# Kernel optimization log

Hardware: AMD Instinct MI355X
Metric: run time of the kernel (lower is better)

The kernel has to match this reference:

```python
import jax, jax.numpy as jnp
import numpy as np

MODEL_DIM = 2048
NUM_HEADS = 16
NUM_KV_HEADS = 4
HEAD_DIM = MODEL_DIM // NUM_HEADS  # 128
ROPE_BASE = 10000.0
LOCAL_WINDOW = 1024
EPS = 1.1920929e-07  # torch.finfo(float32).eps, F.rms_norm default
NEG = -1e30


def setup_inputs() -> dict:
    key = jax.random.key(0)
    ks = jax.random.split(key, 5)
    s = 0.02
    return {
        "x": jax.random.normal(ks[0], (1, 4096, MODEL_DIM), jnp.float32),
        "Wq": jax.random.normal(ks[1], (MODEL_DIM, MODEL_DIM), jnp.float32) * s,
        "Wk": jax.random.normal(ks[2], (NUM_KV_HEADS * HEAD_DIM, MODEL_DIM), jnp.float32) * s,
        "Wv": jax.random.normal(ks[3], (NUM_KV_HEADS * HEAD_DIM, MODEL_DIM), jnp.float32) * s,
        "Wo": jax.random.normal(ks[4], (MODEL_DIM, MODEL_DIM), jnp.float32) * s,
    }


def _rms_norm(x):
    return x * jax.lax.rsqrt(jnp.mean(x * x, axis=-1, keepdims=True) + EPS)


def _rope_tables(seqlen, dtype):
    inv_freq = 1.0 / (ROPE_BASE ** (jnp.arange(0, HEAD_DIM, 2, dtype=jnp.float32) / HEAD_DIM))
    freqs = jnp.arange(seqlen, dtype=jnp.float32)[:, None] * inv_freq[None, :]  # [S, hd/2]
    return jnp.cos(freqs).astype(dtype), jnp.sin(freqs).astype(dtype)


def _apply_rope(x, cos, sin):
    # x: [B, H, S, hd]; cos/sin: [S, hd/2]
    half = x.shape[-1] // 2
    x1, x2 = x[..., :half], x[..., half:]
    c = cos[None, None, :, :]
    s = sin[None, None, :, :]
    return jnp.concatenate((x1 * c + x2 * s, x2 * c - x1 * s), axis=-1)


def reference(x, Wq, Wk, Wv, Wo):
    B, S, _ = x.shape
    G = NUM_HEADS // NUM_KV_HEADS
    q = (x @ Wq.T).reshape(B, S, NUM_HEADS, HEAD_DIM).transpose(0, 2, 1, 3)
    k = (x @ Wk.T).reshape(B, S, NUM_KV_HEADS, HEAD_DIM).transpose(0, 2, 1, 3)
    v = (x @ Wv.T).reshape(B, S, NUM_KV_HEADS, HEAD_DIM).transpose(0, 2, 1, 3)
    q = _rms_norm(q)
    k = _rms_norm(k)
    cos, sin = _rope_tables(S, q.dtype)
    q = _apply_rope(q, cos, sin)
    k = _apply_rope(k, cos, sin)
    # GQA: expand kv heads to match query heads
    k = jnp.repeat(k, G, axis=1)  # [B, H, S, hd]
    v = jnp.repeat(v, G, axis=1)
    scale = 1.0 / np.sqrt(HEAD_DIM)
    scores = jnp.einsum("bhqd,bhkd->bhqk", q, k) * scale  # [B, H, S, S]
    idx = jnp.arange(S)
    causal = idx[None, :] <= idx[:, None]
    in_window = idx[None, :] > idx[:, None] - LOCAL_WINDOW
    allowed = causal & in_window  # [S, S]
    scores = jnp.where(allowed[None, None, :, :], scores, NEG)
    probs = jax.nn.softmax(scores, axis=-1)
    y = jnp.einsum("bhqk,bhkd->bhqd", probs, v)  # [B, H, S, hd]
    y = y.transpose(0, 2, 1, 3).reshape(B, S, MODEL_DIM)
    return y @ Wo.T
```

## Files before the change

kernel.cpp:

```cpp
#include <hip/hip_runtime.h>

typedef short bf16x8 __attribute__((ext_vector_type(8)));
typedef short short4v __attribute__((ext_vector_type(4)));
typedef float f32x4 __attribute__((ext_vector_type(4)));

__device__ __forceinline__ ushort f2b(float f) {
  union { float f; unsigned u; } v; v.f = f;
  unsigned r = v.u + 0x7FFF + ((v.u >> 16) & 1);
  return (ushort)(r >> 16);
}
__device__ __forceinline__ float b2f(ushort u) {
  union { unsigned u; float f; } v; v.u = ((unsigned)u) << 16;
  return v.f;
}
__device__ __forceinline__ unsigned cvtpk(float lo, float hi) {
  unsigned r;
  asm volatile("v_cvt_pk_bf16_f32 %0, %1, %2" : "=v"(r) : "v"(lo), "v"(hi));
  return r;
}
__device__ __forceinline__ f32x4 mfma16(bf16x8 a, bf16x8 b, f32x4 c) {
  return __builtin_amdgcn_mfma_f32_16x16x32_bf16(a, b, c, 0, 0, 0);
}

#define GLD_LDS16(g, l) \
  __builtin_amdgcn_global_load_lds((const __attribute__((address_space(1))) void*)(g), \
                                   (__attribute__((address_space(3))) void*)(l), 16, 0, 0)

__global__ __launch_bounds__(256) void cast_bf16(const float* __restrict__ in,
                                                 ushort* __restrict__ out, int n4) {
  int i = blockIdx.x * 256 + threadIdx.x;
  if (i >= n4) return;
  float4 f = ((const float4*)in)[i];
  ushort4 u;
  u.x = f2b(f.x); u.y = f2b(f.y); u.z = f2b(f.z); u.w = f2b(f.w);
  ((ushort4*)out)[i] = u;
}

__global__ void rope_tables_k(float* __restrict__ cosT, float* __restrict__ sinT) {
  int s = blockIdx.x, i = threadIdx.x;
  float inv = powf(10000.0f, -(float)i * (1.0f / 64.0f));
  float f = (float)s * inv;
  cosT[s * 64 + i] = cosf(f);
  sinT[s * 64 + i] = sinf(f);
}

template <bool BF16OUT>
__global__ __launch_bounds__(256) void gemm_bt(const ushort* __restrict__ A,
                                               const ushort* __restrict__ B,
                                               void* __restrict__ Cout,
                                               int M, int N, int K) {
  __shared__ __align__(16) ushort As[128 * 32];
  __shared__ __align__(16) ushort Bs[128 * 32];
  const int t = threadIdx.x;
  const int lane = t & 63, w = t >> 6;
  const int wr = w >> 1, wc = w & 1;
  const int l15 = lane & 15, l4 = lane >> 4;
  const long m0 = (long)blockIdx.y * 128, n0 = (long)blockIdx.x * 128;
  f32x4 acc[4][4] = {};
  const int srow = t >> 2, scol = (t & 3) * 8;
  const ushort* ga = A + (m0 + srow) * K + scol;
  const ushort* gb = B + (n0 + srow) * K + scol;
  for (int k0 = 0; k0 < K; k0 += 32) {
    GLD_LDS16(ga,          &As[t * 8]);
    GLD_LDS16(ga + 64 * K, &As[2048 + t * 8]);
    GLD_LDS16(gb,          &Bs[t * 8]);
    GLD_LDS16(gb + 64 * K, &Bs[2048 + t * 8]);
    ga += 32; gb += 32;
    asm volatile("s_waitcnt vmcnt(0)" ::: "memory");
    __syncthreads();
    bf16x8 af[4], bfr[4];
#pragma unroll
    for (int i = 0; i < 4; ++i) {
      af[i]  = *(const bf16x8*)(&As[(wr * 64 + i * 16 + l15) * 32 + l4 * 8]);
      bfr[i] = *(const bf16x8*)(&Bs[(wc * 64 + i * 16 + l15) * 32 + l4 * 8]);
    }
#pragma unroll
    for (int i = 0; i < 4; ++i)
#pragma unroll
      for (int j = 0; j < 4; ++j)
        acc[i][j] = mfma16(af[i], bfr[j], acc[i][j]);
    __syncthreads();
  }
#pragma unroll
  for (int i = 0; i < 4; ++i) {
#pragma unroll
    for (int j = 0; j < 4; ++j) {
      long mrow = m0 + wr * 64 + i * 16 + l4 * 4;
      long ncol = n0 + wc * 64 + j * 16 + l15;
#pragma unroll
      for (int r = 0; r < 4; ++r) {
        if constexpr (BF16OUT)
          ((ushort*)Cout)[(mrow + r) * N + ncol] = f2b(acc[i][j][r]);
        else
          ((float*)Cout)[(mrow + r) * N + ncol] = acc[i][j][r];
      }
    }
  }
}

__global__ __launch_bounds__(256) void postproc_k(const ushort* __restrict__ qkvb,
                                                  const float* __restrict__ cosT,
                                                  const float* __restrict__ sinT,
                                                  ushort* __restrict__ qb,
                                                  ushort* __restrict__ kb,
                                                  ushort* __restrict__ vtb) {
  const int lane = threadIdx.x & 63;
  const int s = blockIdx.x * 4 + (threadIdx.x >> 6);
  const int h = blockIdx.y;
  const int colbase = (h < 16) ? h * 128 : (h < 20 ? 2048 + (h - 16) * 128
                                                   : 2560 + (h - 20) * 128);
  const ushort* row = qkvb + (long)s * 3072 + colbase;
  float x1 = b2f(row[lane]), x2 = b2f(row[lane + 64]);
  if (h >= 20) {
    int kvh = h - 20;
    vtb[(long)(kvh * 128 + lane) * 4096 + s]      = f2b(x1);
    vtb[(long)(kvh * 128 + lane + 64) * 4096 + s] = f2b(x2);
    return;
  }
  float ss = x1 * x1 + x2 * x2;
#pragma unroll
  for (int m = 1; m < 64; m <<= 1) ss += __shfl_xor(ss, m);
  float rn = rsqrtf(ss * (1.0f / 128.0f) + 1.1920929e-07f);
  float c = cosT[s * 64 + lane], sn = sinT[s * 64 + lane];
  float x1n = x1 * rn, x2n = x2 * rn;
  float o1 = x1n * c + x2n * sn;
  float o2 = x2n * c - x1n * sn;
  if (h < 16) {
    const float scq = 0.08838834764831845f;
    ushort* dst = qb + ((long)h * 4096 + s) * 128;
    dst[lane] = f2b(o1 * scq);
    dst[lane + 64] = f2b(o2 * scq);
  } else {
    ushort* dst = kb + ((long)(h - 16) * 4096 + s) * 128;
    dst[lane] = f2b(o1);
    dst[lane + 64] = f2b(o2);
  }
}

__global__ __launch_bounds__(512) void attn_k(const ushort* __restrict__ qb,
                                              const ushort* __restrict__ kb,
                                              const ushort* __restrict__ vtb,
                                              ushort* __restrict__ yb) {
  __shared__ __align__(16) ushort lds[32768];
  const int t = threadIdx.x;
  const int lane = t & 63, w = t >> 6;
  const int l15 = lane & 15, l4 = lane >> 4;
  const int q0 = ((int)gridDim.x - 1 - (int)blockIdx.x) * 128;
  const int h = blockIdx.y, kvh = h >> 2;
  const int qw = q0 + w * 16;
  const int q = qw + l15;
  const int swz = l15 & 7;

  const ushort* Qp = qb + ((long)h * 4096 + q) * 128 + l4 * 8;
  bf16x8 qf[4];
#pragma unroll
  for (int c = 0; c < 4; ++c) qf[c] = *(const bf16x8*)(Qp + c * 32);

  const ushort* Kg = kb + (long)kvh * 4096 * 128;
  const ushort* Vg = vtb + (long)kvh * 128 * 4096;

  int kb_lo = q0 - 1023; if (kb_lo < 0) kb_lo = 0; kb_lo &= ~63;
  const int nt = (q0 + 127 - kb_lo) / 64 + 1;

  const int lbuA = (0 * 8 + w) * 512 + lane * 8;
  const int lbuB = (1 * 8 + w) * 512 + lane * 8;
  const int krA = lbuA >> 7, kcA = ((lbuA >> 3) & 15) ^ (krA & 7);
  const int krB = lbuB >> 7, kcB = ((lbuB >> 3) & 15) ^ (krB & 7);
  const int vrA = lbuA >> 6, vcA = ((lbuA >> 3) & 7) ^ (vrA & 7);
  const int vrB = lbuB >> 6, vcB = ((lbuB >> 3) & 7) ^ (vrB & 7);

#define STAGE(kbs, b)                                                        \
  do {                                                                       \
    ushort* Kl_ = &lds[(b) * 16384];                                         \
    ushort* Vl_ = &lds[(b) * 16384 + 8192];                                  \
    GLD_LDS16(Kg + (long)((kbs) + krA) * 128 + kcA * 8, Kl_ + lbuA);         \
    GLD_LDS16(Kg + (long)((kbs) + krB) * 128 + kcB * 8, Kl_ + lbuB);         \
    GLD_LDS16(Vg + (long)vrA * 4096 + (kbs) + vcA * 8, Vl_ + lbuA);          \
    GLD_LDS16(Vg + (long)vrB * 4096 + (kbs) + vcB * 8, Vl_ + lbuB);          \
  } while (0)

  f32x4 o[8] = {};
  float mrun = -1e30f, lrun = 0.0f;

  STAGE(kb_lo, 0);
  asm volatile("s_waitcnt vmcnt(0)" ::: "memory");
  __syncthreads();

  for (int ti = 0; ti < nt; ++ti) {
    const int kbs = kb_lo + ti * 64;
    const int cur = ti & 1;
    if (ti + 1 < nt) STAGE(kbs + 64, cur ^ 1);

    if (kbs + 63 >= qw - 1023 && kbs <= qw + 15) {
      const ushort* Kl = &lds[cur * 16384];
      const ushort* Vl = &lds[cur * 16384 + 8192];

      f32x4 sc[4];
#pragma unroll
      for (int st = 0; st < 4; ++st) {
        sc[st] = f32x4{0.f, 0.f, 0.f, 0.f};
        const ushort* kr = Kl + (st * 16 + l15) * 128;
#pragma unroll
        for (int c = 0; c < 4; ++c)
          sc[st] = mfma16(*(const bf16x8*)(kr + (((c * 4 + l4) ^ swz) * 8)), qf[c], sc[st]);
      }

      float s[16];
#pragma unroll
      for (int st = 0; st < 4; ++st)
#pragma unroll
        for (int r = 0; r < 4; ++r) {
          const int ki = kbs + st * 16 + l4 * 4 + r;
          s[st * 4 + r] = (ki <= q && ki > q - 1024) ? sc[st][r] : -1e30f;
        }

      float m0a = fmaxf(fmaxf(s[0], s[1]), fmaxf(s[2], s[3]));
      float m1a = fmaxf(fmaxf(s[4], s[5]), fmaxf(s[6], s[7]));
      float m2a = fmaxf(fmaxf(s[8], s[9]), fmaxf(s[10], s[11]));
      float m3a = fmaxf(fmaxf(s[12], s[13]), fmaxf(s[14], s[15]));
      float mx = fmaxf(fmaxf(m0a, m1a), fmaxf(m2a, m3a));
      mx = fmaxf(mx, __shfl_xor(mx, 16));
      mx = fmaxf(mx, __shfl_xor(mx, 32));

      float mn;
      if (__all(mx <= mrun + 8.0f)) {
        mn = mrun;
      } else {
        mn = fmaxf(mrun, mx);
        const float corr = __expf(mrun - mn);
        mrun = mn;
#pragma unroll
        for (int db = 0; db < 8; ++db)
#pragma unroll
          for (int r = 0; r < 4; ++r) o[db][r] *= corr;
        lrun *= corr;
      }

      float p[16];
#pragma unroll
      for (int j = 0; j < 16; ++j) p[j] = __expf(s[j] - mn);
      float ps = ((p[0] + p[1]) + (p[2] + p[3])) + ((p[4] + p[5]) + (p[6] + p[7]));
      ps += ((p[8] + p[9]) + (p[10] + p[11])) + ((p[12] + p[13]) + (p[14] + p[15]));
      ps += __shfl_xor(ps, 16);
      ps += __shfl_xor(ps, 32);
      lrun += ps;

      union { unsigned u[4]; bf16x8 v; } pa, pb;
      pa.u[0] = cvtpk(p[0], p[1]);   pa.u[1] = cvtpk(p[2], p[3]);
      pa.u[2] = cvtpk(p[4], p[5]);   pa.u[3] = cvtpk(p[6], p[7]);
      pb.u[0] = cvtpk(p[8], p[9]);   pb.u[1] = cvtpk(p[10], p[11]);
      pb.u[2] = cvtpk(p[12], p[13]); pb.u[3] = cvtpk(p[14], p[15]);

      const int co = 4 * (l4 & 1);
      const int c0 = (l4 >> 1) ^ swz, c1 = (2 + (l4 >> 1)) ^ swz;
      const int c2 = (4 + (l4 >> 1)) ^ swz, c3 = (6 + (l4 >> 1)) ^ swz;
#pragma unroll
      for (int db = 0; db < 8; ++db) {
        const ushort* vr = Vl + (db * 16 + l15) * 64;
        short4v a0 = *(const short4v*)(vr + c0 * 8 + co);
        short4v a1 = *(const short4v*)(vr + c1 * 8 + co);
        bf16x8 va = __builtin_shufflevector(a0, a1, 0, 1, 2, 3, 4, 5, 6, 7);
        o[db] = mfma16(va, pa.v, o[db]);
        short4v b0 = *(const short4v*)(vr + c2 * 8 + co);
        short4v b1 = *(const short4v*)(vr + c3 * 8 + co);
        bf16x8 vb = __builtin_shufflevector(b0, b1, 0, 1, 2, 3, 4, 5, 6, 7);
        o[db] = mfma16(vb, pb.v, o[db]);
      }
    }
    __syncthreads();
  }

  const float inv = 1.0f / lrun;
#pragma unroll
  for (int db = 0; db < 8; ++db)
#pragma unroll
    for (int r = 0; r < 4; ++r)
      yb[(long)q * 2048 + h * 128 + db * 16 + l4 * 4 + r] = f2b(o[db][r] * inv);
}

extern "C" void kernel_launch(void* const* d_in, const int* in_sizes, int n_in,
                              void* d_out, int out_size, void* d_ws, size_t ws_size,
                              hipStream_t stream) {
  (void)in_sizes; (void)n_in; (void)out_size; (void)ws_size;
  const float* x  = (const float*)d_in[0];
  const float* Wq = (const float*)d_in[1];
  const float* Wk = (const float*)d_in[2];
  const float* Wv = (const float*)d_in[3];
  const float* Wo = (const float*)d_in[4];
  const long S = 4096;
  ushort* ws   = (ushort*)d_ws;
  ushort* xb   = ws;
  ushort* wqkv = xb + S * 2048;
  ushort* wob  = wqkv + 3072L * 2048;
  ushort* qkvb = wob + 2048L * 2048;
  ushort* qb   = qkvb + S * 3072;
  ushort* kbuf = qb + S * 2048;
  ushort* vtb  = kbuf + 4L * 4096 * 128;
  ushort* yb   = vtb + 4L * 128 * 4096;
  float* cosT  = (float*)(yb + S * 2048);
  float* sinT  = cosT + S * 64;

  cast_bf16<<<dim3(8192), 256, 0, stream>>>(x, xb, (int)(S * 2048 / 4));
  cast_bf16<<<dim3(4096), 256, 0, stream>>>(Wq, wqkv, 2048 * 2048 / 4);
  cast_bf16<<<dim3(1024), 256, 0, stream>>>(Wk, wqkv + 2048L * 2048, 512 * 2048 / 4);
  cast_bf16<<<dim3(1024), 256, 0, stream>>>(Wv, wqkv + 2560L * 2048, 512 * 2048 / 4);
  cast_bf16<<<dim3(4096), 256, 0, stream>>>(Wo, wob, 2048 * 2048 / 4);

  gemm_bt<true><<<dim3(24, 32), 256, 0, stream>>>(xb, wqkv, qkvb, 4096, 3072, 2048);
  rope_tables_k<<<dim3(4096), 64, 0, stream>>>(cosT, sinT);
  postproc_k<<<dim3(1024, 24), 256, 0, stream>>>(qkvb, cosT, sinT, qb, kbuf, vtb);
  attn_k<<<dim3(32, 16), 512, 0, stream>>>(qb, kbuf, vtb, yb);
  gemm_bt<false><<<dim3(16, 32), 256, 0, stream>>>(yb, wob, d_out, 4096, 2048, 2048);
}
```

Baseline: 238.6 us.

## Replace GEMMs with 8-wave pipelined kernel and retile attention LDS layout

Swaps the simple 128x128 GEMM for a 512-thread, 256-wide tiled GEMM. It double-buffers LDS with async global-to-LDS loads interleaved with MFMA phases, uses s_setprio, and remaps workgroups across XCDs. The attention kernel's K/V LDS layout becomes MFMA-fragment-ordered, so fragments load as contiguous 16-byte reads instead of swizzled split loads. V transpose storage is permuted to match, and masking is skipped for fully in-window tiles. This targets GEMM latency stalls and LDS read overhead, at the cost of complex, fragile layout coupling between postproc and attention.

Result: faster. 225.1 us (-5.6%).

```diff
diff --git a/kernel.cpp b/kernel.cpp
--- a/kernel.cpp
+++ b/kernel.cpp
@@ -1,7 +1,6 @@
 #include <hip/hip_runtime.h>
 
 typedef short bf16x8 __attribute__((ext_vector_type(8)));
-typedef short short4v __attribute__((ext_vector_type(4)));
 typedef float f32x4 __attribute__((ext_vector_type(4)));
 
 __device__ __forceinline__ ushort f2b(float f) {
@@ -44,58 +43,124 @@
   sinT[s * 64 + i] = sinf(f);
 }
 
-template <bool BF16OUT>
-__global__ __launch_bounds__(256) void gemm_bt(const ushort* __restrict__ A,
-                                               const ushort* __restrict__ B,
-                                               void* __restrict__ Cout,
-                                               int M, int N, int K) {
-  __shared__ __align__(16) ushort As[128 * 32];
-  __shared__ __align__(16) ushort Bs[128 * 32];
+template <int BM, int BN, bool BF16OUT>
+__global__ __launch_bounds__(512, 2) void gemm8p(const ushort* __restrict__ A,
+                                                 const ushort* __restrict__ B,
+                                                 void* __restrict__ Cout,
+                                                 int M, int N, int K) {
+  constexpr int AF = BM / 64;
+  constexpr int BF = BN / 64;
+  constexpr int MFR = BM / 32;
+  constexpr int LA = BM / 128;
+  constexpr int LB = BN / 128;
+  constexpr int ASZ = BM * 32;
+  constexpr int BSZ = BN * 32;
+  __shared__ __align__(16) ushort lds[4 * (ASZ + BSZ)];
   const int t = threadIdx.x;
   const int lane = t & 63, w = t >> 6;
-  const int wr = w >> 1, wc = w & 1;
+  const int wr = w & 1, wc = w >> 1;
   const int l15 = lane & 15, l4 = lane >> 4;
-  const long m0 = (long)blockIdx.y * 128, n0 = (long)blockIdx.x * 128;
-  f32x4 acc[4][4] = {};
-  const int srow = t >> 2, scol = (t & 3) * 8;
-  const ushort* ga = A + (m0 + srow) * K + scol;
-  const ushort* gb = B + (n0 + srow) * K + scol;
-  for (int k0 = 0; k0 < K; k0 += 32) {
-    GLD_LDS16(ga,          &As[t * 8]);
-    GLD_LDS16(ga + 64 * K, &As[2048 + t * 8]);
-    GLD_LDS16(gb,          &Bs[t * 8]);
-    GLD_LDS16(gb + 64 * K, &Bs[2048 + t * 8]);
-    ga += 32; gb += 32;
-    asm volatile("s_waitcnt vmcnt(0)" ::: "memory");
-    __syncthreads();
-    bf16x8 af[4], bfr[4];
-#pragma unroll
-    for (int i = 0; i < 4; ++i) {
-      af[i]  = *(const bf16x8*)(&As[(wr * 64 + i * 16 + l15) * 32 + l4 * 8]);
-      bfr[i] = *(const bf16x8*)(&Bs[(wc * 64 + i * 16 + l15) * 32 + l4 * 8]);
-    }
-#pragma unroll
-    for (int i = 0; i < 4; ++i)
-#pragma unroll
-      for (int j = 0; j < 4; ++j)
-        acc[i][j] = mfma16(af[i], bfr[j], acc[i][j]);
-    __syncthreads();
-  }
-#pragma unroll
-  for (int i = 0; i < 4; ++i) {
-#pragma unroll
-    for (int j = 0; j < 4; ++j) {
-      long mrow = m0 + wr * 64 + i * 16 + l4 * 4;
-      long ncol = n0 + wc * 64 + j * 16 + l15;
+  const int nbn = N / BN;
+  const int nwg = (int)gridDim.x;
+  int bid = (int)blockIdx.x;
+  bid = (bid & 7) * (nwg >> 3) + (bid >> 3);
+  const long m0 = (long)(bid / nbn) * BM;
+  const long n0 = (long)(bid % nbn) * BN;
+  const int nk = K >> 6;
+  const int rdl = (l4 * 16 + l15) * 8;
+
+  f32x4 acc[MFR][BF] = {};
+  bf16x8 af[AF], bf[BF];
+
+#define STA(tile, ks)                                                          \
+  do {                                                                         \
+    const int tt_ = (tile) < nk ? (tile) : nk - 1;                             \
+    _Pragma("unroll") for (int c = 0; c < LA; ++c) {                           \
+      const int us_ = t * 8 + c * 4096;                                        \
+      const int row_ = (us_ >> 9) * 16 + ((us_ >> 3) & 15);                    \
+      const int col_ = ((us_ >> 7) & 3) * 8;                                   \
+      GLD_LDS16(A + (m0 + row_) * K + tt_ * 64 + (ks) * 32 + col_,             \
+                &lds[(((tile) & 1) * 2 + (ks)) * ASZ + us_]);                  \
+    }                                                                          \
+  } while (0)
+#define STB(tile, ks)                                                          \
+  do {                                                                         \
+    const int tt_ = (tile) < nk ? (tile) : nk - 1;                             \
+    _Pragma("unroll") for (int c = 0; c < LB; ++c) {                           \
+      const int us_ = t * 8 + c * 4096;                                        \
+      const int row_ = (us_ >> 9) * 16 + ((us_ >> 3) & 15);                    \
+      const int col_ = ((us_ >> 7) & 3) * 8;                                   \
+      GLD_LDS16(B + (n0 + row_) * K + tt_ * 64 + (ks) * 32 + col_,             \
+                &lds[4 * ASZ + (((tile) & 1) * 2 + (ks)) * BSZ + us_]);        \
+    }                                                                          \
+  } while (0)
+#define LDA8(slot, ks, mq)                                                     \
+  _Pragma("unroll") for (int a = 0; a < AF; ++a)                               \
+      af[a] = *(const bf16x8*)(&lds[((slot) * 2 + (ks)) * ASZ +                \
+                                    (wr * MFR + (mq) * AF + a) * 512 + rdl]);
+#define LDB8(slot, ks)                                                         \
+  _Pragma("unroll") for (int b = 0; b < BF; ++b)                               \
+      bf[b] = *(const bf16x8*)(&lds[4 * ASZ + ((slot) * 2 + (ks)) * BSZ +      \
+                                    (wc * BF + b) * 512 + rdl]);
+#define VMW()                                                                  \
+  do {                                                                         \
+    if constexpr (LA + 2 * LB == 6)                                            \
+      asm volatile("s_waitcnt vmcnt(6)" ::: "memory");                         \
+    else                                                                       \
+      asm volatile("s_waitcnt vmcnt(5)" ::: "memory");                         \
+  } while (0)
+#define BARMM(mq)                                                              \
+  do {                                                                         \
+    __builtin_amdgcn_s_barrier();                                              \
+    asm volatile("s_waitcnt lgkmcnt(0)" ::: "memory");                         \
+    __builtin_amdgcn_sched_barrier(0);                                         \
+    __builtin_amdgcn_s_setprio(1);                                             \
+    _Pragma("unroll") for (int a = 0; a < AF; ++a)                             \
+        _Pragma("unroll") for (int b = 0; b < BF; ++b)                         \
+            acc[(mq) * AF + a][b] = mfma16(af[a], bf[b], acc[(mq) * AF + a][b]); \
+    __builtin_amdgcn_s_setprio(0);                                             \
+    __builtin_amdgcn_s_barrier();                                              \
+  } while (0)
+
+  STA(0, 0); STB(0, 0); STA(0, 1); STB(0, 1);
+  STA(1, 0); STB(1, 0); STB(1, 1);
+  VMW();
+  __builtin_amdgcn_s_barrier();
+
+  for (int i = 0; i < (nk >> 1); ++i) {
+    const int t1 = 2 * i + 1, t2 = 2 * i + 2, t3 = 2 * i + 3;
+    LDA8(0, 0, 0); LDB8(0, 0); STA(t1, 1);          BARMM(0);
+    LDA8(0, 0, 1);             STB(t2, 0);          BARMM(1);
+    LDA8(0, 1, 0); LDB8(0, 1); STA(t2, 0);          BARMM(0);
+    LDA8(0, 1, 1);             STB(t2, 1); VMW();   BARMM(1);
+    LDA8(1, 0, 0); LDB8(1, 0); STA(t2, 1);          BARMM(0);
+    LDA8(1, 0, 1);             STB(t3, 0);          BARMM(1);
+    LDA8(1, 1, 0); LDB8(1, 1); STA(t3, 0);          BARMM(0);
+    LDA8(1, 1, 1);             STB(t3, 1); VMW();   BARMM(1);
+  }
+  asm volatile("s_waitcnt vmcnt(0)" ::: "memory");
+
+#pragma unroll
+  for (int m = 0; m < MFR; ++m) {
+#pragma unroll
+    for (int n = 0; n < BF; ++n) {
+      long mrow = m0 + wr * (BM / 2) + m * 16 + l4 * 4;
+      long ncol = n0 + wc * (BN / 4) + n * 16 + l15;
 #pragma unroll
       for (int r = 0; r < 4; ++r) {
         if constexpr (BF16OUT)
-          ((ushort*)Cout)[(mrow + r) * N + ncol] = f2b(acc[i][j][r]);
+          ((ushort*)Cout)[(mrow + r) * N + ncol] = f2b(acc[m][n][r]);
         else
-          ((float*)Cout)[(mrow + r) * N + ncol] = acc[i][j][r];
+          ((float*)Cout)[(mrow + r) * N + ncol] = acc[m][n][r];
       }
     }
   }
+#undef STA
+#undef STB
+#undef LDA8
+#undef LDB8
+#undef VMW
+#undef BARMM
 }
 
 __global__ __launch_bounds__(256) void postproc_k(const ushort* __restrict__ qkvb,
@@ -113,8 +178,9 @@
   float x1 = b2f(row[lane]), x2 = b2f(row[lane + 64]);
   if (h >= 20) {
     int kvh = h - 20;
-    vtb[(long)(kvh * 128 + lane) * 4096 + s]      = f2b(x1);
-    vtb[(long)(kvh * 128 + lane + 64) * 4096 + s] = f2b(x2);
+    int spos = (s & ~31) | (((s >> 2) & 3) * 8 + ((s >> 4) & 1) * 4 + (s & 3));
+    vtb[(long)(kvh * 128 + lane) * 4096 + spos]      = f2b(x1);
+    vtb[(long)(kvh * 128 + lane + 64) * 4096 + spos] = f2b(x2);
     return;
   }
   float ss = x1 * x1 + x2 * x2;
@@ -149,7 +215,6 @@
   const int h = blockIdx.y, kvh = h >> 2;
   const int qw = q0 + w * 16;
   const int q = qw + l15;
-  const int swz = l15 & 7;
 
   const ushort* Qp = qb + ((long)h * 4096 + q) * 128 + l4 * 8;
   bf16x8 qf[4];
@@ -162,21 +227,25 @@
   int kb_lo = q0 - 1023; if (kb_lo < 0) kb_lo = 0; kb_lo &= ~63;
   const int nt = (q0 + 127 - kb_lo) / 64 + 1;
 
-  const int lbuA = (0 * 8 + w) * 512 + lane * 8;
-  const int lbuB = (1 * 8 + w) * 512 + lane * 8;
-  const int krA = lbuA >> 7, kcA = ((lbuA >> 3) & 15) ^ (krA & 7);
-  const int krB = lbuB >> 7, kcB = ((lbuB >> 3) & 15) ^ (krB & 7);
-  const int vrA = lbuA >> 6, vcA = ((lbuA >> 3) & 7) ^ (vrA & 7);
-  const int vrB = lbuB >> 6, vcB = ((lbuB >> 3) & 7) ^ (vrB & 7);
+  const int lbuA = w * 512 + lane * 8;
+  const int lbuB = lbuA + 4096;
+  const int krA = ((lbuA >> 9) >> 2) * 16 + ((lbuA >> 3) & 15);
+  const int kcA = ((lbuA >> 9) & 3) * 32 + ((lbuA >> 7) & 3) * 8;
+  const int krB = ((lbuB >> 9) >> 2) * 16 + ((lbuB >> 3) & 15);
+  const int kcB = ((lbuB >> 9) & 3) * 32 + ((lbuB >> 7) & 3) * 8;
+  const int vrA = ((lbuA >> 9) >> 1) * 16 + ((lbuA >> 5) & 15);
+  const int vcA = ((lbuA >> 9) & 1) * 32 + ((lbuA >> 3) & 3) * 8;
+  const int vrB = ((lbuB >> 9) >> 1) * 16 + ((lbuB >> 5) & 15);
+  const int vcB = ((lbuB >> 9) & 1) * 32 + ((lbuB >> 3) & 3) * 8;
 
 #define STAGE(kbs, b)                                                        \
   do {                                                                       \
     ushort* Kl_ = &lds[(b) * 16384];                                         \
     ushort* Vl_ = &lds[(b) * 16384 + 8192];                                  \
-    GLD_LDS16(Kg + (long)((kbs) + krA) * 128 + kcA * 8, Kl_ + lbuA);         \
-    GLD_LDS16(Kg + (long)((kbs) + krB) * 128 + kcB * 8, Kl_ + lbuB);         \
-    GLD_LDS16(Vg + (long)vrA * 4096 + (kbs) + vcA * 8, Vl_ + lbuA);          \
-    GLD_LDS16(Vg + (long)vrB * 4096 + (kbs) + vcB * 8, Vl_ + lbuB);          \
+    GLD_LDS16(Kg + (long)((kbs) + krA) * 128 + kcA, Kl_ + lbuA);             \
+    GLD_LDS16(Kg + (long)((kbs) + krB) * 128 + kcB, Kl_ + lbuB);             \
+    GLD_LDS16(Vg + (long)vrA * 4096 + (kbs) + vcA, Vl_ + lbuA);              \
+    GLD_LDS16(Vg + (long)vrB * 4096 + (kbs) + vcB, Vl_ + lbuB);              \
   } while (0)
 
   f32x4 o[8] = {};
@@ -194,25 +263,34 @@
     if (kbs + 63 >= qw - 1023 && kbs <= qw + 15) {
       const ushort* Kl = &lds[cur * 16384];
       const ushort* Vl = &lds[cur * 16384 + 8192];
+      const int rdl = (l4 * 16 + l15) * 8;
 
       f32x4 sc[4];
 #pragma unroll
       for (int st = 0; st < 4; ++st) {
         sc[st] = f32x4{0.f, 0.f, 0.f, 0.f};
-        const ushort* kr = Kl + (st * 16 + l15) * 128;
 #pragma unroll
         for (int c = 0; c < 4; ++c)
-          sc[st] = mfma16(*(const bf16x8*)(kr + (((c * 4 + l4) ^ swz) * 8)), qf[c], sc[st]);
-      }
-
+          sc[st] = mfma16(*(const bf16x8*)(Kl + (st * 4 + c) * 512 + rdl),
+                          qf[c], sc[st]);
+      }
+
+      const bool full = (kbs + 64 <= qw) && (kbs >= qw - 1008);
       float s[16];
-#pragma unroll
-      for (int st = 0; st < 4; ++st)
-#pragma unroll
-        for (int r = 0; r < 4; ++r) {
-          const int ki = kbs + st * 16 + l4 * 4 + r;
-          s[st * 4 + r] = (ki <= q && ki > q - 1024) ? sc[st][r] : -1e30f;
-        }
+      if (full) {
+#pragma unroll
+        for (int st = 0; st < 4; ++st)
+#pragma unroll
+          for (int r = 0; r < 4; ++r) s[st * 4 + r] = sc[st][r];
+      } else {
+#pragma unroll
+        for (int st = 0; st < 4; ++st)
+#pragma unroll
+          for (int r = 0; r < 4; ++r) {
+            const int ki = kbs + st * 16 + l4 * 4 + r;
+            s[st * 4 + r] = (ki <= q && ki > q - 1024) ? sc[st][r] : -1e30f;
+          }
+      }
 
       float m0a = fmaxf(fmaxf(s[0], s[1]), fmaxf(s[2], s[3]));
       float m1a = fmaxf(fmaxf(s[4], s[5]), fmaxf(s[6], s[7]));
@@ -251,20 +329,12 @@
       pb.u[0] = cvtpk(p[8], p[9]);   pb.u[1] = cvtpk(p[10], p[11]);
       pb.u[2] = cvtpk(p[12], p[13]); pb.u[3] = cvtpk(p[14], p[15]);
 
-      const int co = 4 * (l4 & 1);
-      const int c0 = (l4 >> 1) ^ swz, c1 = (2 + (l4 >> 1)) ^ swz;
-      const int c2 = (4 + (l4 >> 1)) ^ swz, c3 = (6 + (l4 >> 1)) ^ swz;
+      const int vbase = l15 * 32 + l4 * 8;
 #pragma unroll
       for (int db = 0; db < 8; ++db) {
-        const ushort* vr = Vl + (db * 16 + l15) * 64;
-        short4v a0 = *(const short4v*)(vr + c0 * 8 + co);
-        short4v a1 = *(const short4v*)(vr + c1 * 8 + co);
-        bf16x8 va = __builtin_shufflevector(a0, a1, 0, 1, 2, 3, 4, 5, 6, 7);
-        o[db] = mfma16(va, pa.v, o[db]);
-        short4v b0 = *(const short4v*)(vr + c2 * 8 + co);
-        short4v b1 = *(const short4v*)(vr + c3 * 8 + co);
-        bf16x8 vb = __builtin_shufflevector(b0, b1, 0, 1, 2, 3, 4, 5, 6, 7);
-        o[db] = mfma16(vb, pb.v, o[db]);
+        const ushort* vrp = Vl + db * 1024 + vbase;
+        o[db] = mfma16(*(const bf16x8*)vrp, pa.v, o[db]);
+        o[db] = mfma16(*(const bf16x8*)(vrp + 512), pb.v, o[db]);
       }
     }
     __syncthreads();
@@ -306,9 +376,9 @@
   cast_bf16<<<dim3(1024), 256, 0, stream>>>(Wv, wqkv + 2560L * 2048, 512 * 2048 / 4);
   cast_bf16<<<dim3(4096), 256, 0, stream>>>(Wo, wob, 2048 * 2048 / 4);
 
-  gemm_bt<true><<<dim3(24, 32), 256, 0, stream>>>(xb, wqkv, qkvb, 4096, 3072, 2048);
+  gemm8p<256, 256, true><<<dim3(192), 512, 0, stream>>>(xb, wqkv, qkvb, 4096, 3072, 2048);
   rope_tables_k<<<dim3(4096), 64, 0, stream>>>(cosT, sinT);
   postproc_k<<<dim3(1024, 24), 256, 0, stream>>>(qkvb, cosT, sinT, qb, kbuf, vtb);
   attn_k<<<dim3(32, 16), 512, 0, stream>>>(qb, kbuf, vtb, yb);
-  gemm_bt<false><<<dim3(16, 32), 256, 0, stream>>>(yb, wob, d_out, 4096, 2048, 2048);
-}
+  gemm8p<128, 256, false><<<dim3(256), 512, 0, stream>>>(yb, wob, d_out, 4096, 2048, 2048);
+}
```
